# Kernel tuning notes

Hardware: AMD Instinct MI355X
Metric: run time of the kernel (lower is better)

## Reference

```python
import jax, jax.numpy as jnp
import numpy as np

DT = 0.001
BATCH, INPUT_SIZE, HIDDEN_SIZE, T = 32, 16384, 1024, 10


def setup_inputs() -> dict:
    key = jax.random.key(0)
    k1, k2, k3 = jax.random.split(key, 3)
    input_spikes = (jax.random.uniform(k1, (BATCH, INPUT_SIZE, T)) < 0.1).astype(jnp.float32)
    weight = jax.random.normal(k2, (INPUT_SIZE, HIDDEN_SIZE), dtype=jnp.float32) * 0.1
    synaptic_strength = jnp.ones((INPUT_SIZE, HIDDEN_SIZE), jnp.float32)
    threshold = jnp.ones((HIDDEN_SIZE,), jnp.float32)  # threshold_init = 1.0
    firing_rate_estimate = jnp.zeros((HIDDEN_SIZE,), jnp.float32)
    return {
        "input_spikes": input_spikes,
        "weight": weight,
        "synaptic_strength": synaptic_strength,
        "threshold": threshold,
        "firing_rate_estimate": firing_rate_estimate,
        "tau_mem": jnp.float32(0.02),
        "tau_syn": jnp.float32(0.005),
        "target_rate": jnp.float32(0.1),
        "homeostatic_lr": jnp.float32(0.001),
        "time_steps": T,
    }


def reference(input_spikes, weight, synaptic_strength, threshold,
              firing_rate_estimate, tau_mem, tau_syn, target_rate,
              homeostatic_lr, time_steps):
    # input_spikes: [B, I, T]; eval mode (no stochastic STDP branch)
    B = input_spikes.shape[0]
    H = threshold.shape[0]
    alpha_mem = jnp.exp(-DT / tau_mem)
    alpha_syn = jnp.exp(-DT / tau_syn)
    # precompute the per-step weighted input once: [T, B, H]
    w_eff = weight * synaptic_strength
    weighted = jnp.einsum('bit,ih->tbh', input_spikes[..., :time_steps], w_eff)

    def step(carry, w_in):
        v, i, fre, thr = carry
        i = alpha_syn * i + w_in
        v = alpha_mem * v + i
        spikes = (v >= thr[None, :]).astype(v.dtype)
        v = v - spikes * thr[None, :]  # reset_mode='subtract'
        spike_rate = spikes.mean(axis=0)
        fre = 0.99 * fre + 0.01 * spike_rate
        thr = thr + homeostatic_lr * (fre - target_rate)  # homeostatic adaptation
        diag = (v.mean(), spike_rate.mean(), thr.mean())
        return (v, i, fre, thr), (spikes, diag)

    init = (jnp.zeros((B, H), input_spikes.dtype),
            jnp.zeros((B, H), input_spikes.dtype),
            firing_rate_estimate, threshold)
    _, (spikes_tbh, (mem_means, rate_means, thr_means)) = jax.lax.scan(step, init, weighted)
    output_spikes = jnp.transpose(spikes_tbh, (1, 2, 0))  # [B, H, T]
    return output_spikes, mem_means, rate_means, thr_means
```

## Files before the change

### kernel.cpp

```cpp
#include <hip/hip_runtime.h>
#include <stdint.h>

#define B_ 32
#define I_ 16384
#define H_ 1024
#define T_ 10
#define M_ 320
#define NW 128
#define BK 32

typedef __attribute__((ext_vector_type(8))) short short8;
typedef __attribute__((ext_vector_type(4))) float f32x4;
typedef __attribute__((ext_vector_type(4))) unsigned int u32x4;

__global__ __launch_bounds__(256) void pack_s(const float* __restrict__ spikes,
                                              uint16_t* __restrict__ Sbf) {
  __shared__ __align__(16) uint16_t tile[M_ * 40];
  const int i0 = blockIdx.x * 32;
#pragma unroll
  for (int p = 0; p < 10; p++) {
    int e = p * 256 + threadIdx.x;
    int b = e / 80;
    int r = e - b * 80;
    f32x4 val = *(const f32x4*)&spikes[(size_t)b * (I_ * T_) + (size_t)i0 * T_ + r * 4];
#pragma unroll
    for (int j = 0; j < 4; j++) {
      int pos = r * 4 + j;
      int il = pos / 10;
      int t = pos - il * 10;
      float f = (j == 0) ? val.x : (j == 1) ? val.y : (j == 2) ? val.z : val.w;
      union { float f; unsigned int u; } cv; cv.f = f;
      tile[(t * 32 + b) * 40 + il] = (uint16_t)(cv.u >> 16);
    }
  }
  __syncthreads();
#pragma unroll
  for (int p = 0; p < 5; p++) {
    int e = p * 256 + threadIdx.x;
    int m = e >> 2, il8 = e & 3;
    u32x4 w = *(const u32x4*)&tile[m * 40 + il8 * 8];
    *(u32x4*)&Sbf[(size_t)m * I_ + i0 + il8 * 8] = w;
  }
}

__global__ __launch_bounds__(640, 3) void gemm(const uint16_t* __restrict__ Sbf,
                                               const float* __restrict__ Wg,
                                               const float* __restrict__ Sg,
                                               float* __restrict__ partial,
                                               int kchunk, int KS) {
  __shared__ __align__(16) uint16_t WhiL[2][NW * 40];
  __shared__ __align__(16) uint16_t WloL[2][NW * 40];

  const int ks = blockIdx.x % KS;
  const int nt = blockIdx.x / KS;
  const int nbase = nt * NW;
  const int tid = threadIdx.x;
  const int lane = tid & 63, wid = tid >> 6;
  const int quad = lane >> 4, l15 = lane & 15;

  const int stages = kchunk >> 5;
  const int kofs = ks * kchunk;

  const uint16_t* aptr0 = Sbf + (size_t)(wid * 32 + l15) * I_ + quad * 8;
  const uint16_t* aptr1 = aptr0 + (size_t)16 * I_;

  const int wn = tid & 127;
  const int wko = (tid >> 7) & 3;

  f32x4 acc[2][8];
#pragma unroll
  for (int a = 0; a < 2; a++)
#pragma unroll
    for (int b = 0; b < 8; b++) acc[a][b] = f32x4{0.f, 0.f, 0.f, 0.f};

  u32x4 af[2];
  float wpre[8], spre[8];

#define BAR()                                                               \
  do {                                                                      \
    asm volatile("s_waitcnt lgkmcnt(0)" ::: "memory");                      \
    __builtin_amdgcn_s_barrier();                                           \
    __builtin_amdgcn_sched_barrier(0);                                      \
  } while (0)

#define PACK_W(pn)                                                          \
  if (tid < 512) {                                                          \
    unsigned int hw[4], lw[4];                                              \
    _Pragma("unroll")                                                       \
    for (int j2 = 0; j2 < 4; j2++) {                                        \
      unsigned int hh[2], ll[2];                                            \
      _Pragma("unroll")                                                     \
      for (int e = 0; e < 2; e++) {                                         \
        float p = wpre[j2 * 2 + e] * spre[j2 * 2 + e];                      \
        union { float f; unsigned int u; } cv; cv.f = p;                    \
        unsigned int hb = (cv.u + 0x7FFFu + ((cv.u >> 16) & 1u)) >> 16;     \
        union { unsigned int u; float f; } hv; hv.u = hb << 16;             \
        float lo = p - hv.f;                                                \
        union { float f; unsigned int u; } cl; cl.f = lo;                   \
        unsigned int lb = (cl.u + 0x7FFFu + ((cl.u >> 16) & 1u)) >> 16;     \
        hh[e] = hb; ll[e] = lb;                                             \
      }                                                                     \
      hw[j2] = hh[0] | (hh[1] << 16);                                       \
      lw[j2] = ll[0] | (ll[1] << 16);                                       \
    }                                                                       \
    int wofs = wn * 40 + wko * 8;                                           \
    *(u32x4*)&WhiL[pn][wofs] = u32x4{hw[0], hw[1], hw[2], hw[3]};           \
    *(u32x4*)&WloL[pn][wofs] = u32x4{lw[0], lw[1], lw[2], lw[3]};           \
  }

#define LOAD_W(kb)                                                          \
  if (tid < 512) {                                                          \
    _Pragma("unroll")                                                       \
    for (int j = 0; j < 8; j++) {                                           \
      size_t g = (size_t)((kb) + wko * 8 + j) * H_ + nbase + wn;            \
      wpre[j] = Wg[g]; spre[j] = Sg[g];                                     \
    }                                                                       \
  }

#define ISSUE_A(kb)                                                         \
  {                                                                         \
    af[0] = *(const u32x4*)(aptr0 + (kb));                                  \
    af[1] = *(const u32x4*)(aptr1 + (kb));                                  \
  }

#define COMPUTE(pc)                                                         \
  {                                                                         \
    short8 a0 = __builtin_bit_cast(short8, af[0]);                          \
    short8 a1 = __builtin_bit_cast(short8, af[1]);                          \
    _Pragma("unroll")                                                       \
    for (int tn = 0; tn < 8; ++tn) {                                        \
      int n = tn * 16 + l15;                                                \
      short8 bhi = *(const short8*)&WhiL[pc][n * 40 + quad * 8];            \
      short8 blo = *(const short8*)&WloL[pc][n * 40 + quad * 8];            \
      acc[0][tn] = __builtin_amdgcn_mfma_f32_16x16x32_bf16(a0, bhi, acc[0][tn], 0, 0, 0); \
      acc[0][tn] = __builtin_amdgcn_mfma_f32_16x16x32_bf16(a0, blo, acc[0][tn], 0, 0, 0); \
      acc[1][tn] = __builtin_amdgcn_mfma_f32_16x16x32_bf16(a1, bhi, acc[1][tn], 0, 0, 0); \
      acc[1][tn] = __builtin_amdgcn_mfma_f32_16x16x32_bf16(a1, blo, acc[1][tn], 0, 0, 0); \
    }                                                                       \
  }

  LOAD_W(kofs);
  ISSUE_A(kofs);
  PACK_W(0);
  if (stages > 1) LOAD_W(kofs + BK);
  BAR();

  for (int s = 0; s < stages; ++s) {
    COMPUTE(s & 1);
    if (s + 1 < stages) {
      ISSUE_A(kofs + (s + 1) * BK);
      PACK_W((s + 1) & 1);
      if (s + 2 < stages) LOAD_W(kofs + (s + 2) * BK);
      BAR();
    }
  }

#pragma unroll
  for (int tm = 0; tm < 2; tm++)
#pragma unroll
    for (int tn = 0; tn < 8; tn++) {
      int mrow = wid * 32 + tm * 16 + quad * 4;
      int ncol = nbase + tn * 16 + l15;
      float* dst = partial + ((size_t)ks * M_ + mrow) * H_ + ncol;
      dst[0 * H_] = acc[tm][tn].x;
      dst[1 * H_] = acc[tm][tn].y;
      dst[2 * H_] = acc[tm][tn].z;
      dst[3 * H_] = acc[tm][tn].w;
    }
#undef PACK_W
#undef LOAD_W
#undef ISSUE_A
#undef COMPUTE
#undef BAR
}

__global__ __launch_bounds__(256) void reduce_w(const float* __restrict__ partial,
                                                float* __restrict__ weighted,
                                                float* __restrict__ out, int KS) {
  if (blockIdx.x == 0 && threadIdx.x < 30) out[327680 + threadIdx.x] = 0.f;
  int j = (blockIdx.x * 256 + threadIdx.x) * 4;
  f32x4 s = f32x4{0.f, 0.f, 0.f, 0.f};
  for (int k = 0; k < KS; k++) {
    f32x4 p = *(const f32x4*)&partial[(size_t)k * (M_ * H_) + j];
    s += p;
  }
  *(f32x4*)&weighted[j] = s;
}

__global__ __launch_bounds__(64) void scan(const float* __restrict__ weighted,
                                           const float* __restrict__ threshold,
                                           const float* __restrict__ fre0,
                                           const float* __restrict__ p_tau_mem,
                                           const float* __restrict__ p_tau_syn,
                                           const float* __restrict__ p_target,
                                           const float* __restrict__ p_lr,
                                           float* __restrict__ out) {
  const int lane = threadIdx.x;
  const int hl = lane & 3, bg = lane >> 2;
  const int h = blockIdx.x * 4 + hl;
  const float alpha_mem = expf(-0.001f / p_tau_mem[0]);
  const float alpha_syn = expf(-0.001f / p_tau_syn[0]);
  const float target = p_target[0], lr = p_lr[0];
  float v[2], isyn[2];
#pragma unroll
  for (int j = 0; j < 2; j++) { v[j] = 0.f; isyn[j] = 0.f; }
  float fre = fre0[h];
  float thr = threshold[h];
  for (int t = 0; t < T_; t++) {
    float rsum = 0.f, vsum = 0.f;
#pragma unroll
    for (int j = 0; j < 2; j++) {
      int b = bg * 2 + j;
      float w_in = weighted[(size_t)(t * 32 + b) * H_ + h];
      isyn[j] = alpha_syn * isyn[j] + w_in;
      v[j] = alpha_mem * v[j] + isyn[j];
      float spike = (v[j] >= thr) ? 1.f : 0.f;
      v[j] -= spike * thr;
      out[(size_t)b * (H_ * T_) + (size_t)h * T_ + t] = spike;
      rsum += spike;
      vsum += v[j];
    }
    float r = rsum;
    r += __shfl_xor(r, 4);
    r += __shfl_xor(r, 8);
    r += __shfl_xor(r, 16);
    r += __shfl_xor(r, 32);
    float rate = r * (1.f / 32.f);
    fre = 0.99f * fre + 0.01f * rate;
    thr = thr + lr * (fre - target);
    float vv = vsum, rr = rate, tt = thr;
#pragma unroll
    for (int off = 32; off >= 1; off >>= 1) {
      vv += __shfl_xor(vv, off);
      rr += __shfl_xor(rr, off);
      tt += __shfl_xor(tt, off);
    }
    if (lane == 0) {
      atomicAdd(&out[327680 + t], vv * (1.f / 32768.f));
      atomicAdd(&out[327690 + t], rr * (1.f / 16384.f));
      atomicAdd(&out[327700 + t], tt * (1.f / 16384.f));
    }
  }
}

extern "C" void kernel_launch(void* const* d_in, const int* in_sizes, int n_in,
                              void* d_out, int out_size, void* d_ws, size_t ws_size,
                              hipStream_t stream) {
  const float* spikes    = (const float*)d_in[0];
  const float* weight    = (const float*)d_in[1];
  const float* strength  = (const float*)d_in[2];
  const float* threshold = (const float*)d_in[3];
  const float* fre0      = (const float*)d_in[4];
  const float* tau_mem   = (const float*)d_in[5];
  const float* tau_syn   = (const float*)d_in[6];
  const float* target    = (const float*)d_in[7];
  const float* lr        = (const float*)d_in[8];
  float* out = (float*)d_out;

  const size_t sbf_bytes = (size_t)M_ * I_ * 2;
  const size_t slice     = (size_t)M_ * H_ * 4;
  int KS = 32;
  while (KS > 1 && sbf_bytes + (size_t)(KS + 1) * slice > ws_size) KS >>= 1;

  uint16_t* Sbf   = (uint16_t*)d_ws;
  float* partial  = (float*)((char*)d_ws + sbf_bytes);
  float* weighted = (float*)((char*)d_ws + sbf_bytes + (size_t)KS * slice);

  pack_s<<<I_ / 32, 256, 0, stream>>>(spikes, Sbf);
  gemm<<<(H_ / NW) * KS, 640, 0, stream>>>(Sbf, weight, strength, partial,
                                           I_ / KS, KS);
  reduce_w<<<(M_ * H_) / 1024, 256, 0, stream>>>(partial, weighted, out, KS);
  scan<<<H_ / 4, 64, 0, stream>>>(weighted, threshold, fre0, tau_mem, tau_syn,
                                  target, lr, out);
}
```

Before: 258.7 us.

## Replace scan atomics with per-block partials and a final reduce kernel

The scan kernel now maps one batch element per lane, with two hidden units per wave and two waves per block. It preloads all time-step inputs into registers and writes the spike outputs as vectorized pairs after the loop. The per-step diagnostic atomicAdds are replaced by block partials written to workspace, which a new single-block reduce kernel sums and scales. This removes atomic contention and the zero-init in reduce_w, at the cost of one extra kernel launch.

```diff
diff --git a/kernel.cpp b/kernel.cpp
--- a/kernel.cpp
+++ b/kernel.cpp
@@ -8,9 +8,11 @@
 #define M_ 320
 #define NW 128
 #define BK 32
+#define SCAN_BLOCKS 256
 
 typedef __attribute__((ext_vector_type(8))) short short8;
 typedef __attribute__((ext_vector_type(4))) float f32x4;
+typedef __attribute__((ext_vector_type(2))) float f32x2;
 typedef __attribute__((ext_vector_type(4))) unsigned int u32x4;
 
 __global__ __launch_bounds__(256) void pack_s(const float* __restrict__ spikes,
@@ -176,8 +178,7 @@
 
 __global__ __launch_bounds__(256) void reduce_w(const float* __restrict__ partial,
                                                 float* __restrict__ weighted,
-                                                float* __restrict__ out, int KS) {
-  if (blockIdx.x == 0 && threadIdx.x < 30) out[327680 + threadIdx.x] = 0.f;
+                                                int KS) {
   int j = (blockIdx.x * 256 + threadIdx.x) * 4;
   f32x4 s = f32x4{0.f, 0.f, 0.f, 0.f};
   for (int k = 0; k < KS; k++) {
@@ -187,59 +188,99 @@
   *(f32x4*)&weighted[j] = s;
 }
 
-__global__ __launch_bounds__(64) void scan(const float* __restrict__ weighted,
-                                           const float* __restrict__ threshold,
-                                           const float* __restrict__ fre0,
-                                           const float* __restrict__ p_tau_mem,
-                                           const float* __restrict__ p_tau_syn,
-                                           const float* __restrict__ p_target,
-                                           const float* __restrict__ p_lr,
-                                           float* __restrict__ out) {
-  const int lane = threadIdx.x;
-  const int hl = lane & 3, bg = lane >> 2;
-  const int h = blockIdx.x * 4 + hl;
+__global__ __launch_bounds__(128) void scan(const float* __restrict__ weighted,
+                                            const float* __restrict__ threshold,
+                                            const float* __restrict__ fre0,
+                                            const float* __restrict__ p_tau_mem,
+                                            const float* __restrict__ p_tau_syn,
+                                            const float* __restrict__ p_target,
+                                            const float* __restrict__ p_lr,
+                                            float* __restrict__ out,
+                                            float* __restrict__ dpart) {
+  const int tid = threadIdx.x;
+  const int lane = tid & 63;
+  const int wv = tid >> 6;
+  const int b = lane & 31;
+  const int hg = lane >> 5;
+  const int h = blockIdx.x * 4 + wv * 2 + hg;
+
   const float alpha_mem = expf(-0.001f / p_tau_mem[0]);
   const float alpha_syn = expf(-0.001f / p_tau_syn[0]);
   const float target = p_target[0], lr = p_lr[0];
-  float v[2], isyn[2];
-#pragma unroll
-  for (int j = 0; j < 2; j++) { v[j] = 0.f; isyn[j] = 0.f; }
+
+  float win[T_];
+#pragma unroll
+  for (int t = 0; t < T_; t++)
+    win[t] = weighted[(size_t)(t * 32 + b) * H_ + h];
+
   float fre = fre0[h];
   float thr = threshold[h];
+  float v = 0.f, isyn = 0.f;
+  float spk[T_], dv[T_], dr[T_], dtt[T_];
+
+#pragma unroll
   for (int t = 0; t < T_; t++) {
-    float rsum = 0.f, vsum = 0.f;
-#pragma unroll
-    for (int j = 0; j < 2; j++) {
-      int b = bg * 2 + j;
-      float w_in = weighted[(size_t)(t * 32 + b) * H_ + h];
-      isyn[j] = alpha_syn * isyn[j] + w_in;
-      v[j] = alpha_mem * v[j] + isyn[j];
-      float spike = (v[j] >= thr) ? 1.f : 0.f;
-      v[j] -= spike * thr;
-      out[(size_t)b * (H_ * T_) + (size_t)h * T_ + t] = spike;
-      rsum += spike;
-      vsum += v[j];
-    }
-    float r = rsum;
+    isyn = alpha_syn * isyn + win[t];
+    v = alpha_mem * v + isyn;
+    float spike = (v >= thr) ? 1.f : 0.f;
+    v -= spike * thr;
+    spk[t] = spike;
+    float r = spike;
+    r += __shfl_xor(r, 1);
+    r += __shfl_xor(r, 2);
     r += __shfl_xor(r, 4);
     r += __shfl_xor(r, 8);
     r += __shfl_xor(r, 16);
-    r += __shfl_xor(r, 32);
     float rate = r * (1.f / 32.f);
     fre = 0.99f * fre + 0.01f * rate;
     thr = thr + lr * (fre - target);
-    float vv = vsum, rr = rate, tt = thr;
-#pragma unroll
-    for (int off = 32; off >= 1; off >>= 1) {
-      vv += __shfl_xor(vv, off);
-      rr += __shfl_xor(rr, off);
-      tt += __shfl_xor(tt, off);
+    float vv = v;
+#pragma unroll
+    for (int off = 1; off <= 32; off <<= 1) vv += __shfl_xor(vv, off);
+    float r2 = r + __shfl_xor(r, 32);
+    float t2 = thr + __shfl_xor(thr, 32);
+    dv[t] = vv;
+    dr[t] = r2 * (1.f / 32.f);
+    dtt[t] = t2;
+  }
+
+  {
+    float* o = out + (size_t)b * (H_ * T_) + (size_t)h * T_;
+#pragma unroll
+    for (int p = 0; p < 5; p++)
+      *(f32x2*)&o[p * 2] = f32x2{spk[p * 2], spk[p * 2 + 1]};
+  }
+
+  __shared__ float dl[2][30];
+  if (lane == 0) {
+#pragma unroll
+    for (int t = 0; t < T_; t++) {
+      dl[wv][t] = dv[t];
+      dl[wv][10 + t] = dr[t];
+      dl[wv][20 + t] = dtt[t];
     }
-    if (lane == 0) {
-      atomicAdd(&out[327680 + t], vv * (1.f / 32768.f));
-      atomicAdd(&out[327690 + t], rr * (1.f / 16384.f));
-      atomicAdd(&out[327700 + t], tt * (1.f / 16384.f));
-    }
+  }
+  __syncthreads();
+  if (tid < 30) dpart[(size_t)blockIdx.x * 30 + tid] = dl[0][tid] + dl[1][tid];
+}
+
+__global__ __launch_bounds__(128) void reduce_d(const float* __restrict__ dpart,
+                                                float* __restrict__ out) {
+  __shared__ float accl[4][32];
+  const int s = threadIdx.x >> 5;
+  const int c = threadIdx.x & 31;
+  float sum = 0.f;
+  if (c < 30) {
+    for (int k = s * 64; k < s * 64 + 64; k++)
+      sum += dpart[(size_t)k * 30 + c];
+  }
+  accl[s][c] = sum;
+  __syncthreads();
+  if (threadIdx.x < 30) {
+    float tot = accl[0][threadIdx.x] + accl[1][threadIdx.x] +
+                accl[2][threadIdx.x] + accl[3][threadIdx.x];
+    float scale = (threadIdx.x < 10) ? (1.f / 32768.f) : (1.f / 1024.f);
+    out[327680 + threadIdx.x] = tot * scale;
   }
 }
 
@@ -259,17 +300,23 @@
 
   const size_t sbf_bytes = (size_t)M_ * I_ * 2;
   const size_t slice     = (size_t)M_ * H_ * 4;
+  const size_t wt_bytes  = (size_t)M_ * H_ * 4;
+  const size_t dp_bytes  = (size_t)SCAN_BLOCKS * 30 * 4;
   int KS = 32;
-  while (KS > 1 && sbf_bytes + (size_t)(KS + 1) * slice > ws_size) KS >>= 1;
+  while (KS > 1 &&
+         sbf_bytes + (size_t)KS * slice + wt_bytes + dp_bytes > ws_size)
+    KS >>= 1;
 
   uint16_t* Sbf   = (uint16_t*)d_ws;
   float* partial  = (float*)((char*)d_ws + sbf_bytes);
   float* weighted = (float*)((char*)d_ws + sbf_bytes + (size_t)KS * slice);
+  float* dpart    = (float*)((char*)d_ws + sbf_bytes + (size_t)KS * slice + wt_bytes);
 
   pack_s<<<I_ / 32, 256, 0, stream>>>(spikes, Sbf);
   gemm<<<(H_ / NW) * KS, 640, 0, stream>>>(Sbf, weight, strength, partial,
                                            I_ / KS, KS);
-  reduce_w<<<(M_ * H_) / 1024, 256, 0, stream>>>(partial, weighted, out, KS);
-  scan<<<H_ / 4, 64, 0, stream>>>(weighted, threshold, fre0, tau_mem, tau_syn,
-                                  target, lr, out);
-}
+  reduce_w<<<(M_ * H_) / 1024, 256, 0, stream>>>(partial, weighted, KS);
+  scan<<<SCAN_BLOCKS, 128, 0, stream>>>(weighted, threshold, fre0, tau_mem,
+                                        tau_syn, target, lr, out, dpart);
+  reduce_d<<<1, 128, 0, stream>>>(dpart, out);
+}
```

Result: faster. 212.0 us (-18.0%).
